# Optimization experiments

Measured on AMD Instinct MI355X. Metric: run time of the kernel, lower is better.

## Reference

```python
import jax, jax.numpy as jnp
import numpy as np

ALPHA = 0.2          # LeakyReLU negative slope
NEG_INF = -9e15      # mask value used by the original module
B, L, D, F_IN, F_OUT = 16, 256, 128, 64, 64


def setup_inputs() -> dict:
    key = jax.random.key(0)
    k1, k2, k3, k4 = jax.random.split(key, 4)
    h = jax.random.normal(k1, (B, L, D, F_IN), dtype=jnp.float32)
    adj = jax.random.randint(k2, (B, L, D, D), 0, 2, dtype=jnp.int32)
    # xavier_uniform(gain=1.414) bounds
    bW = 1.414 * np.sqrt(6.0 / (F_IN + F_OUT))
    W = jax.random.uniform(k3, (F_IN, F_OUT), dtype=jnp.float32, minval=-bW, maxval=bW)
    ba = 1.414 * np.sqrt(6.0 / (2 * F_OUT + 1))
    a = jax.random.uniform(k4, (2 * F_OUT, 1), dtype=jnp.float32, minval=-ba, maxval=ba)
    return {"h": h, "adj": adj, "W": W, "a": a}


def reference(h, adj, W, a):
    # h: [B,L,D,F_in], adj: [B,L,D,D]
    Wh = jnp.einsum('bldf,fo->bldo', h, W)              # [B,L,D,F_out]
    a1 = a[:F_OUT, 0]                                    # dots the "source" node i
    a2 = a[F_OUT:, 0]                                    # dots the "target" node j
    e_i = Wh @ a1                                        # [B,L,D]
    e_j = Wh @ a2                                        # [B,L,D]
    e = e_i[..., :, None] + e_j[..., None, :]            # [B,L,D,D] pairwise scores
    e = jnp.where(e > 0, e, ALPHA * e)                   # LeakyReLU
    att = jnp.where(adj > 0, e, NEG_INF)
    att = jax.nn.softmax(att, axis=-1)                   # dropout=eval mode (no-op)
    h_prime = jnp.einsum('bldk,blko->bldo', att, Wh)     # [B,L,D,F_out]
    return h_prime
```

## Files before the change

### kernel.cpp

```cpp
#include <hip/hip_runtime.h>

constexpr int D_   = 128;
constexpr int FIN  = 64;
constexpr int FOUT = 64;
constexpr float ALPHA = 0.2f;

typedef _Float16 f16x8 __attribute__((ext_vector_type(8)));
typedef float    f32x4 __attribute__((ext_vector_type(4)));

__global__ __launch_bounds__(256, 4) void gat_kernel(
    const float* __restrict__ hg, const int* __restrict__ adjg,
    const float* __restrict__ Wg, const float* __restrict__ ag,
    float* __restrict__ outg)
{
    __shared__ __align__(16) unsigned short sX[128 * 64];
    __shared__ __align__(16) unsigned short sPt[64 * 64];
    __shared__ __align__(16) float sA[2 * FOUT];
    __shared__ float sEi[D_];
    __shared__ __align__(16) float sEj[D_];
    __shared__ float sL[D_];
    __shared__ float sMxW[4];

    const int tid  = threadIdx.x;
    const int lane = tid & 63;
    const int w    = tid >> 6;
    const int g    = lane >> 4;
    const int m16  = lane & 15;

    const long bl = blockIdx.x;
    const float* hp   = hg   + bl * (long)(D_ * FIN);
    const int*   adjp = adjg + bl * (long)(D_ * D_);
    float*       outp = outg + bl * (long)(D_ * FOUT);

    char* xb = (char*)sX;
    char* pb = (char*)sPt;

    {
        const float4* h4 = (const float4*)hp;
        #pragma unroll
        for (int k = 0; k < 8; ++k) {
            int idx = tid + 256 * k;
            float4 v = h4[idx];
            int row = idx >> 4;
            int f   = (idx & 15) << 2;
            union { _Float16 h[4]; uint2 u; } cv;
            cv.h[0] = (_Float16)v.x; cv.h[1] = (_Float16)v.y;
            cv.h[2] = (_Float16)v.z; cv.h[3] = (_Float16)v.w;
            int off = (row * 128 + f * 2) ^ ((row & 7) << 4);
            *(uint2*)(xb + off) = cv.u;
        }
        {
            const int f0 = (tid & 15) * 4;
            const int o0 = (tid >> 4) * 4;
            float4 r0 = *(const float4*)&Wg[(f0 + 0) * 64 + o0];
            float4 r1 = *(const float4*)&Wg[(f0 + 1) * 64 + o0];
            float4 r2 = *(const float4*)&Wg[(f0 + 2) * 64 + o0];
            float4 r3 = *(const float4*)&Wg[(f0 + 3) * 64 + o0];
            float col[4][4] = {{r0.x, r1.x, r2.x, r3.x},
                               {r0.y, r1.y, r2.y, r3.y},
                               {r0.z, r1.z, r2.z, r3.z},
                               {r0.w, r1.w, r2.w, r3.w}};
            #pragma unroll
            for (int c = 0; c < 4; ++c) {
                int o = o0 + c;
                union { _Float16 h[4]; uint2 u; } cv;
                cv.h[0] = (_Float16)col[c][0]; cv.h[1] = (_Float16)col[c][1];
                cv.h[2] = (_Float16)col[c][2]; cv.h[3] = (_Float16)col[c][3];
                int off = (o * 128 + f0 * 2) ^ ((o & 7) << 4);
                *(uint2*)(pb + off) = cv.u;
            }
        }
        if (tid < 2 * FOUT) sA[tid] = ag[tid];
    }

    const int row0 = w * 32 + m16;
    const int* aprow0 = adjp + row0 * D_ + g * 8;
    const int* aprow1 = aprow0 + 16 * D_;
    int4 areg[4];
    areg[0] = *(const int4*)(aprow0);
    areg[1] = *(const int4*)(aprow0 + 4);
    areg[2] = *(const int4*)(aprow1);
    areg[3] = *(const int4*)(aprow1 + 4);
    __syncthreads();

    f32x4 acc[2][4];
    #pragma unroll
    for (int mt = 0; mt < 2; ++mt)
        #pragma unroll
        for (int nt = 0; nt < 4; ++nt) acc[mt][nt] = (f32x4){0.f, 0.f, 0.f, 0.f};

    #pragma unroll
    for (int kt = 0; kt < 2; ++kt) {
        f16x8 af[2], bf[4];
        #pragma unroll
        for (int mt = 0; mt < 2; ++mt) {
            int row = w * 32 + mt * 16 + m16;
            af[mt] = *(const f16x8*)(xb + ((row * 128 + kt * 64 + g * 16) ^ ((row & 7) << 4)));
        }
        #pragma unroll
        for (int nt = 0; nt < 4; ++nt) {
            int o = nt * 16 + m16;
            bf[nt] = *(const f16x8*)(pb + ((o * 128 + kt * 64 + g * 16) ^ ((o & 7) << 4)));
        }
        #pragma unroll
        for (int mt = 0; mt < 2; ++mt)
            #pragma unroll
            for (int nt = 0; nt < 4; ++nt)
                acc[mt][nt] = __builtin_amdgcn_mfma_f32_16x16x32_f16(af[mt], bf[nt], acc[mt][nt], 0, 0, 0);
    }
    __syncthreads();

    {
        float a1v[4], a2v[4];
        #pragma unroll
        for (int nt = 0; nt < 4; ++nt) {
            a1v[nt] = sA[nt * 16 + m16];
            a2v[nt] = sA[FOUT + nt * 16 + m16];
        }
        float wmax = -3.0e38f;
        #pragma unroll
        for (int mt = 0; mt < 2; ++mt) {
            #pragma unroll
            for (int r = 0; r < 4; ++r) {
                float ei = 0.f, ej = 0.f;
                #pragma unroll
                for (int nt = 0; nt < 4; ++nt) {
                    float v = acc[mt][nt][r];
                    ei += v * a1v[nt];
                    ej += v * a2v[nt];
                }
                #pragma unroll
                for (int s = 1; s < 16; s <<= 1) {
                    ei += __shfl_xor(ei, s);
                    ej += __shfl_xor(ej, s);
                }
                int row = w * 32 + mt * 16 + g * 4 + r;
                if (m16 == 0) { sEi[row] = ei; sEj[row] = ej; }
                wmax = fmaxf(wmax, ej);
            }
        }
        wmax = fmaxf(wmax, __shfl_xor(wmax, 16));
        wmax = fmaxf(wmax, __shfl_xor(wmax, 32));
        if (lane == 0) sMxW[w] = wmax;

        #pragma unroll
        for (int mt = 0; mt < 2; ++mt) {
            int j0r = w * 32 + mt * 16 + g * 4;
            #pragma unroll
            for (int nt = 0; nt < 4; ++nt) {
                int o = nt * 16 + m16;
                union { _Float16 h[4]; uint2 u; } cv;
                cv.h[0] = (_Float16)acc[mt][nt][0];
                cv.h[1] = (_Float16)acc[mt][nt][1];
                cv.h[2] = (_Float16)acc[mt][nt][2];
                cv.h[3] = (_Float16)acc[mt][nt][3];
                int off = (o * 256 + j0r * 2) ^ ((o & 7) << 4);
                *(uint2*)(xb + off) = cv.u;
            }
        }
    }
    __syncthreads();

    #pragma unroll
    for (int mt = 0; mt < 2; ++mt)
        #pragma unroll
        for (int nt = 0; nt < 4; ++nt) acc[mt][nt] = (f32x4){0.f, 0.f, 0.f, 0.f};

    const float ei0 = sEi[row0];
    const float ei1 = sEi[row0 + 16];
    const float mxj = fmaxf(fmaxf(sMxW[0], sMxW[1]), fmaxf(sMxW[2], sMxW[3]));
    float t0 = ei0 + mxj, t1 = ei1 + mxj;
    const float mi0 = t0 > 0.f ? t0 : ALPHA * t0;
    const float mi1 = t1 > 0.f ? t1 : ALPHA * t1;
    float lp0 = 0.f, lp1 = 0.f;

    #pragma unroll
    for (int jt = 0; jt < 4; ++jt) {
        const int j0 = jt * 32;
        float4 ejA = *(const float4*)&sEj[j0 + g * 8];
        float4 ejB = *(const float4*)&sEj[j0 + g * 8 + 4];
        float ejv[8] = {ejA.x, ejA.y, ejA.z, ejA.w, ejB.x, ejB.y, ejB.z, ejB.w};
        int aa0[8] = {areg[0].x, areg[0].y, areg[0].z, areg[0].w,
                      areg[1].x, areg[1].y, areg[1].z, areg[1].w};
        int aa1[8] = {areg[2].x, areg[2].y, areg[2].z, areg[2].w,
                      areg[3].x, areg[3].y, areg[3].z, areg[3].w};
        f16x8 pa0, pa1;
        #pragma unroll
        for (int q = 0; q < 8; ++q) {
            float e0 = ei0 + ejv[q];
            e0 = e0 > 0.f ? e0 : ALPHA * e0;
            float p0 = (aa0[q] > 0) ? __expf(e0 - mi0) : 0.f;
            lp0 += p0;
            pa0[q] = (_Float16)p0;
            float e1 = ei1 + ejv[q];
            e1 = e1 > 0.f ? e1 : ALPHA * e1;
            float p1 = (aa1[q] > 0) ? __expf(e1 - mi1) : 0.f;
            lp1 += p1;
            pa1[q] = (_Float16)p1;
        }
        if (jt < 3) {
            const int* n0 = aprow0 + (jt + 1) * 32;
            const int* n1 = aprow1 + (jt + 1) * 32;
            areg[0] = *(const int4*)(n0);
            areg[1] = *(const int4*)(n0 + 4);
            areg[2] = *(const int4*)(n1);
            areg[3] = *(const int4*)(n1 + 4);
        }

        f16x8 wb[4];
        #pragma unroll
        for (int nt = 0; nt < 4; ++nt) {
            int o = nt * 16 + m16;
            wb[nt] = *(const f16x8*)(xb + ((o * 256 + j0 * 2 + g * 16) ^ ((o & 7) << 4)));
        }
        #pragma unroll
        for (int nt = 0; nt < 4; ++nt) {
            acc[0][nt] = __builtin_amdgcn_mfma_f32_16x16x32_f16(pa0, wb[nt], acc[0][nt], 0, 0, 0);
            acc[1][nt] = __builtin_amdgcn_mfma_f32_16x16x32_f16(pa1, wb[nt], acc[1][nt], 0, 0, 0);
        }
    }

    lp0 += __shfl_xor(lp0, 16); lp0 += __shfl_xor(lp0, 32);
    lp1 += __shfl_xor(lp1, 16); lp1 += __shfl_xor(lp1, 32);
    if (g == 0) {
        sL[row0]      = lp0;
        sL[row0 + 16] = lp1;
    }

    #pragma unroll
    for (int mtx = 0; mtx < 2; ++mtx) {
        #pragma unroll
        for (int r = 0; r < 4; ++r) {
            int row = w * 32 + mtx * 16 + g * 4 + r;
            float inv = 1.0f / sL[row];
            #pragma unroll
            for (int nt = 0; nt < 4; ++nt)
                outp[row * 64 + nt * 16 + m16] = acc[mtx][nt][r] * inv;
        }
    }
}

extern "C" void kernel_launch(void* const* d_in, const int* in_sizes, int n_in,
                              void* d_out, int out_size, void* d_ws, size_t ws_size,
                              hipStream_t stream) {
    const float* h   = (const float*)d_in[0];
    const int*   adj = (const int*)d_in[1];
    const float* W   = (const float*)d_in[2];
    const float* a   = (const float*)d_in[3];
    float*       out = (float*)d_out;
    gat_kernel<<<dim3(16 * 256), dim3(256), 0, stream>>>(h, adj, W, a, out);
}
```

Before: 476.0 us.

## Process two (b,l) slices per block with double-buffered h prefetch

Each block now handles two consecutive (b,l) slices, halving the grid. The second slice's h tile is loaded into registers during the first slice's projection, and its adjacency row fragment is prefetched at the end of the first softmax/aggregation phase. W is converted once and shared across both slices. The cost is an extra 16KB of LDS, which may lower occupancy, more register pressure from holding the h prefetch, and fewer blocks to balance across CUs.

```diff
diff --git a/kernel.cpp b/kernel.cpp
--- a/kernel.cpp
+++ b/kernel.cpp
@@ -13,7 +13,8 @@
     const float* __restrict__ Wg, const float* __restrict__ ag,
     float* __restrict__ outg)
 {
-    __shared__ __align__(16) unsigned short sX[128 * 64];
+    __shared__ __align__(16) unsigned short sX0[128 * 64];
+    __shared__ __align__(16) unsigned short sX1[128 * 64];
     __shared__ __align__(16) unsigned short sPt[64 * 64];
     __shared__ __align__(16) float sA[2 * FOUT];
     __shared__ float sEi[D_];
@@ -26,17 +27,26 @@
     const int w    = tid >> 6;
     const int g    = lane >> 4;
     const int m16  = lane & 15;
-
-    const long bl = blockIdx.x;
-    const float* hp   = hg   + bl * (long)(D_ * FIN);
-    const int*   adjp = adjg + bl * (long)(D_ * D_);
-    float*       outp = outg + bl * (long)(D_ * FOUT);
-
-    char* xb = (char*)sX;
-    char* pb = (char*)sPt;
+    const int row0 = w * 32 + m16;
+
+    const long bl0 = 2 * (long)blockIdx.x;
+    const long bl1 = bl0 + 1;
+    const float* hp0   = hg   + bl0 * (long)(D_ * FIN);
+    const float* hp1   = hg   + bl1 * (long)(D_ * FIN);
+    const int*   adjp0 = adjg + bl0 * (long)(D_ * D_);
+    const int*   adjp1 = adjg + bl1 * (long)(D_ * D_);
+    float*       outp0 = outg + bl0 * (long)(D_ * FOUT);
+    float*       outp1 = outg + bl1 * (long)(D_ * FOUT);
+
+    char* xb0 = (char*)sX0;
+    char* xb1 = (char*)sX1;
+    char* pb  = (char*)sPt;
+
+    f32x4 acc[2][4];
+    int4  areg[4];
 
     {
-        const float4* h4 = (const float4*)hp;
+        const float4* h4 = (const float4*)hp0;
         #pragma unroll
         for (int k = 0; k < 8; ++k) {
             int idx = tid + 256 * k;
@@ -47,70 +57,63 @@
             cv.h[0] = (_Float16)v.x; cv.h[1] = (_Float16)v.y;
             cv.h[2] = (_Float16)v.z; cv.h[3] = (_Float16)v.w;
             int off = (row * 128 + f * 2) ^ ((row & 7) << 4);
-            *(uint2*)(xb + off) = cv.u;
-        }
-        {
-            const int f0 = (tid & 15) * 4;
-            const int o0 = (tid >> 4) * 4;
-            float4 r0 = *(const float4*)&Wg[(f0 + 0) * 64 + o0];
-            float4 r1 = *(const float4*)&Wg[(f0 + 1) * 64 + o0];
-            float4 r2 = *(const float4*)&Wg[(f0 + 2) * 64 + o0];
-            float4 r3 = *(const float4*)&Wg[(f0 + 3) * 64 + o0];
-            float col[4][4] = {{r0.x, r1.x, r2.x, r3.x},
-                               {r0.y, r1.y, r2.y, r3.y},
-                               {r0.z, r1.z, r2.z, r3.z},
-                               {r0.w, r1.w, r2.w, r3.w}};
-            #pragma unroll
-            for (int c = 0; c < 4; ++c) {
-                int o = o0 + c;
-                union { _Float16 h[4]; uint2 u; } cv;
-                cv.h[0] = (_Float16)col[c][0]; cv.h[1] = (_Float16)col[c][1];
-                cv.h[2] = (_Float16)col[c][2]; cv.h[3] = (_Float16)col[c][3];
-                int off = (o * 128 + f0 * 2) ^ ((o & 7) << 4);
-                *(uint2*)(pb + off) = cv.u;
-            }
+            *(uint2*)(xb0 + off) = cv.u;
+        }
+        const int f0 = (tid & 15) * 4;
+        const int o0 = (tid >> 4) * 4;
+        float4 r0 = *(const float4*)&Wg[(f0 + 0) * 64 + o0];
+        float4 r1 = *(const float4*)&Wg[(f0 + 1) * 64 + o0];
+        float4 r2 = *(const float4*)&Wg[(f0 + 2) * 64 + o0];
+        float4 r3 = *(const float4*)&Wg[(f0 + 3) * 64 + o0];
+        float col[4][4] = {{r0.x, r1.x, r2.x, r3.x},
+                           {r0.y, r1.y, r2.y, r3.y},
+                           {r0.z, r1.z, r2.z, r3.z},
+                           {r0.w, r1.w, r2.w, r3.w}};
+        #pragma unroll
+        for (int c = 0; c < 4; ++c) {
+            int o = o0 + c;
+            union { _Float16 h[4]; uint2 u; } cv;
+            cv.h[0] = (_Float16)col[c][0]; cv.h[1] = (_Float16)col[c][1];
+            cv.h[2] = (_Float16)col[c][2]; cv.h[3] = (_Float16)col[c][3];
+            int off = (o * 128 + f0 * 2) ^ ((o & 7) << 4);
+            *(uint2*)(pb + off) = cv.u;
         }
         if (tid < 2 * FOUT) sA[tid] = ag[tid];
+        const int* a0 = adjp0 + row0 * D_ + g * 8;
+        areg[0] = *(const int4*)(a0);
+        areg[1] = *(const int4*)(a0 + 4);
+        areg[2] = *(const int4*)(a0 + 16 * D_);
+        areg[3] = *(const int4*)(a0 + 16 * D_ + 4);
     }
-
-    const int row0 = w * 32 + m16;
-    const int* aprow0 = adjp + row0 * D_ + g * 8;
-    const int* aprow1 = aprow0 + 16 * D_;
-    int4 areg[4];
-    areg[0] = *(const int4*)(aprow0);
-    areg[1] = *(const int4*)(aprow0 + 4);
-    areg[2] = *(const int4*)(aprow1);
-    areg[3] = *(const int4*)(aprow1 + 4);
-    __syncthreads();
-
-    f32x4 acc[2][4];
-    #pragma unroll
-    for (int mt = 0; mt < 2; ++mt)
-        #pragma unroll
-        for (int nt = 0; nt < 4; ++nt) acc[mt][nt] = (f32x4){0.f, 0.f, 0.f, 0.f};
-
-    #pragma unroll
-    for (int kt = 0; kt < 2; ++kt) {
-        f16x8 af[2], bf[4];
-        #pragma unroll
-        for (int mt = 0; mt < 2; ++mt) {
-            int row = w * 32 + mt * 16 + m16;
-            af[mt] = *(const f16x8*)(xb + ((row * 128 + kt * 64 + g * 16) ^ ((row & 7) << 4)));
-        }
-        #pragma unroll
-        for (int nt = 0; nt < 4; ++nt) {
-            int o = nt * 16 + m16;
-            bf[nt] = *(const f16x8*)(pb + ((o * 128 + kt * 64 + g * 16) ^ ((o & 7) << 4)));
-        }
+    __syncthreads();
+
+    auto phaseA = [&](char* xb) {
         #pragma unroll
         for (int mt = 0; mt < 2; ++mt)
             #pragma unroll
-            for (int nt = 0; nt < 4; ++nt)
-                acc[mt][nt] = __builtin_amdgcn_mfma_f32_16x16x32_f16(af[mt], bf[nt], acc[mt][nt], 0, 0, 0);
-    }
-    __syncthreads();
-
-    {
+            for (int nt = 0; nt < 4; ++nt) acc[mt][nt] = (f32x4){0.f, 0.f, 0.f, 0.f};
+        #pragma unroll
+        for (int kt = 0; kt < 2; ++kt) {
+            f16x8 af[2], bf[4];
+            #pragma unroll
+            for (int mt = 0; mt < 2; ++mt) {
+                int row = w * 32 + mt * 16 + m16;
+                af[mt] = *(const f16x8*)(xb + ((row * 128 + kt * 64 + g * 16) ^ ((row & 7) << 4)));
+            }
+            #pragma unroll
+            for (int nt = 0; nt < 4; ++nt) {
+                int o = nt * 16 + m16;
+                bf[nt] = *(const f16x8*)(pb + ((o * 128 + kt * 64 + g * 16) ^ ((o & 7) << 4)));
+            }
+            #pragma unroll
+            for (int mt = 0; mt < 2; ++mt)
+                #pragma unroll
+                for (int nt = 0; nt < 4; ++nt)
+                    acc[mt][nt] = __builtin_amdgcn_mfma_f32_16x16x32_f16(af[mt], bf[nt], acc[mt][nt], 0, 0, 0);
+        }
+    };
+
+    auto phaseB = [&](char* xb) {
         float a1v[4], a2v[4];
         #pragma unroll
         for (int nt = 0; nt < 4; ++nt) {
@@ -142,7 +145,6 @@
         wmax = fmaxf(wmax, __shfl_xor(wmax, 16));
         wmax = fmaxf(wmax, __shfl_xor(wmax, 32));
         if (lane == 0) sMxW[w] = wmax;
-
         #pragma unroll
         for (int mt = 0; mt < 2; ++mt) {
             int j0r = w * 32 + mt * 16 + g * 4;
@@ -158,86 +160,121 @@
                 *(uint2*)(xb + off) = cv.u;
             }
         }
+    };
+
+    auto phaseC = [&](char* xb, const int* adjp, float* outp, const int* adjp_next) {
+        #pragma unroll
+        for (int mt = 0; mt < 2; ++mt)
+            #pragma unroll
+            for (int nt = 0; nt < 4; ++nt) acc[mt][nt] = (f32x4){0.f, 0.f, 0.f, 0.f};
+        const float ei0 = sEi[row0];
+        const float ei1 = sEi[row0 + 16];
+        const float mxj = fmaxf(fmaxf(sMxW[0], sMxW[1]), fmaxf(sMxW[2], sMxW[3]));
+        float t0 = ei0 + mxj, t1 = ei1 + mxj;
+        const float mi0 = t0 > 0.f ? t0 : ALPHA * t0;
+        const float mi1 = t1 > 0.f ? t1 : ALPHA * t1;
+        float lp0 = 0.f, lp1 = 0.f;
+        const int* aprow0 = adjp + row0 * D_ + g * 8;
+        const int* aprow1 = aprow0 + 16 * D_;
+        #pragma unroll
+        for (int jt = 0; jt < 4; ++jt) {
+            const int j0 = jt * 32;
+            float4 ejA = *(const float4*)&sEj[j0 + g * 8];
+            float4 ejB = *(const float4*)&sEj[j0 + g * 8 + 4];
+            float ejv[8] = {ejA.x, ejA.y, ejA.z, ejA.w, ejB.x, ejB.y, ejB.z, ejB.w};
+            int aa0[8] = {areg[0].x, areg[0].y, areg[0].z, areg[0].w,
+                          areg[1].x, areg[1].y, areg[1].z, areg[1].w};
+            int aa1[8] = {areg[2].x, areg[2].y, areg[2].z, areg[2].w,
+                          areg[3].x, areg[3].y, areg[3].z, areg[3].w};
+            f16x8 pa0, pa1;
+            #pragma unroll
+            for (int q = 0; q < 8; ++q) {
+                float e0 = ei0 + ejv[q];
+                e0 = e0 > 0.f ? e0 : ALPHA * e0;
+                float p0 = (aa0[q] > 0) ? __expf(e0 - mi0) : 0.f;
+                lp0 += p0;
+                pa0[q] = (_Float16)p0;
+                float e1 = ei1 + ejv[q];
+                e1 = e1 > 0.f ? e1 : ALPHA * e1;
+                float p1 = (aa1[q] > 0) ? __expf(e1 - mi1) : 0.f;
+                lp1 += p1;
+                pa1[q] = (_Float16)p1;
+            }
+            if (jt < 3) {
+                const int* n0 = aprow0 + (jt + 1) * 32;
+                const int* n1 = aprow1 + (jt + 1) * 32;
+                areg[0] = *(const int4*)(n0);
+                areg[1] = *(const int4*)(n0 + 4);
+                areg[2] = *(const int4*)(n1);
+                areg[3] = *(const int4*)(n1 + 4);
+            } else if (adjp_next) {
+                const int* n0 = adjp_next + row0 * D_ + g * 8;
+                areg[0] = *(const int4*)(n0);
+                areg[1] = *(const int4*)(n0 + 4);
+                areg[2] = *(const int4*)(n0 + 16 * D_);
+                areg[3] = *(const int4*)(n0 + 16 * D_ + 4);
+            }
+            f16x8 wb[4];
+            #pragma unroll
+            for (int nt = 0; nt < 4; ++nt) {
+                int o = nt * 16 + m16;
+                wb[nt] = *(const f16x8*)(xb + ((o * 256 + j0 * 2 + g * 16) ^ ((o & 7) << 4)));
+            }
+            #pragma unroll
+            for (int nt = 0; nt < 4; ++nt) {
+                acc[0][nt] = __builtin_amdgcn_mfma_f32_16x16x32_f16(pa0, wb[nt], acc[0][nt], 0, 0, 0);
+                acc[1][nt] = __builtin_amdgcn_mfma_f32_16x16x32_f16(pa1, wb[nt], acc[1][nt], 0, 0, 0);
+            }
+        }
+        lp0 += __shfl_xor(lp0, 16); lp0 += __shfl_xor(lp0, 32);
+        lp1 += __shfl_xor(lp1, 16); lp1 += __shfl_xor(lp1, 32);
+        if (g == 0) {
+            sL[row0]      = lp0;
+            sL[row0 + 16] = lp1;
+        }
+        #pragma unroll
+        for (int mtx = 0; mtx < 2; ++mtx) {
+            #pragma unroll
+            for (int r = 0; r < 4; ++r) {
+                int row = w * 32 + mtx * 16 + g * 4 + r;
+                float inv = 1.0f / sL[row];
+                #pragma unroll
+                for (int nt = 0; nt < 4; ++nt)
+                    outp[row * 64 + nt * 16 + m16] = acc[mtx][nt][r] * inv;
+            }
+        }
+    };
+
+    phaseA(xb0);
+    float4 hreg[8];
+    {
+        const float4* h4 = (const float4*)hp1;
+        #pragma unroll
+        for (int k = 0; k < 8; ++k) hreg[k] = h4[tid + 256 * k];
     }
     __syncthreads();
-
+    phaseB(xb0);
     #pragma unroll
-    for (int mt = 0; mt < 2; ++mt)
-        #pragma unroll
-        for (int nt = 0; nt < 4; ++nt) acc[mt][nt] = (f32x4){0.f, 0.f, 0.f, 0.f};
-
-    const float ei0 = sEi[row0];
-    const float ei1 = sEi[row0 + 16];
-    const float mxj = fmaxf(fmaxf(sMxW[0], sMxW[1]), fmaxf(sMxW[2], sMxW[3]));
-    float t0 = ei0 + mxj, t1 = ei1 + mxj;
-    const float mi0 = t0 > 0.f ? t0 : ALPHA * t0;
-    const float mi1 = t1 > 0.f ? t1 : ALPHA * t1;
-    float lp0 = 0.f, lp1 = 0.f;
-
-    #pragma unroll
-    for (int jt = 0; jt < 4; ++jt) {
-        const int j0 = jt * 32;
-        float4 ejA = *(const float4*)&sEj[j0 + g * 8];
-        float4 ejB = *(const float4*)&sEj[j0 + g * 8 + 4];
-        float ejv[8] = {ejA.x, ejA.y, ejA.z, ejA.w, ejB.x, ejB.y, ejB.z, ejB.w};
-        int aa0[8] = {areg[0].x, areg[0].y, areg[0].z, areg[0].w,
-                      areg[1].x, areg[1].y, areg[1].z, areg[1].w};
-        int aa1[8] = {areg[2].x, areg[2].y, areg[2].z, areg[2].w,
-                      areg[3].x, areg[3].y, areg[3].z, areg[3].w};
-        f16x8 pa0, pa1;
-        #pragma unroll
-        for (int q = 0; q < 8; ++q) {
-            float e0 = ei0 + ejv[q];
-            e0 = e0 > 0.f ? e0 : ALPHA * e0;
-            float p0 = (aa0[q] > 0) ? __expf(e0 - mi0) : 0.f;
-            lp0 += p0;
-            pa0[q] = (_Float16)p0;
-            float e1 = ei1 + ejv[q];
-            e1 = e1 > 0.f ? e1 : ALPHA * e1;
-            float p1 = (aa1[q] > 0) ? __expf(e1 - mi1) : 0.f;
-            lp1 += p1;
-            pa1[q] = (_Float16)p1;
-        }
-        if (jt < 3) {
-            const int* n0 = aprow0 + (jt + 1) * 32;
-            const int* n1 = aprow1 + (jt + 1) * 32;
-            areg[0] = *(const int4*)(n0);
-            areg[1] = *(const int4*)(n0 + 4);
-            areg[2] = *(const int4*)(n1);
-            areg[3] = *(const int4*)(n1 + 4);
-        }
-
-        f16x8 wb[4];
-        #pragma unroll
-        for (int nt = 0; nt < 4; ++nt) {
-            int o = nt * 16 + m16;
-            wb[nt] = *(const f16x8*)(xb + ((o * 256 + j0 * 2 + g * 16) ^ ((o & 7) << 4)));
-        }
-        #pragma unroll
-        for (int nt = 0; nt < 4; ++nt) {
-            acc[0][nt] = __builtin_amdgcn_mfma_f32_16x16x32_f16(pa0, wb[nt], acc[0][nt], 0, 0, 0);
-            acc[1][nt] = __builtin_amdgcn_mfma_f32_16x16x32_f16(pa1, wb[nt], acc[1][nt], 0, 0, 0);
-        }
+    for (int k = 0; k < 8; ++k) {
+        int idx = tid + 256 * k;
+        float4 v = hreg[k];
+        int row = idx >> 4;
+        int f   = (idx & 15) << 2;
+        union { _Float16 h[4]; uint2 u; } cv;
+        cv.h[0] = (_Float16)v.x; cv.h[1] = (_Float16)v.y;
+        cv.h[2] = (_Float16)v.z; cv.h[3] = (_Float16)v.w;
+        int off = (row * 128 + f * 2) ^ ((row & 7) << 4);
+        *(uint2*)(xb1 + off) = cv.u;
     }
-
-    lp0 += __shfl_xor(lp0, 16); lp0 += __shfl_xor(lp0, 32);
-    lp1 += __shfl_xor(lp1, 16); lp1 += __shfl_xor(lp1, 32);
-    if (g == 0) {
-        sL[row0]      = lp0;
-        sL[row0 + 16] = lp1;
-    }
-
-    #pragma unroll
-    for (int mtx = 0; mtx < 2; ++mtx) {
-        #pragma unroll
-        for (int r = 0; r < 4; ++r) {
-            int row = w * 32 + mtx * 16 + g * 4 + r;
-            float inv = 1.0f / sL[row];
-            #pragma unroll
-            for (int nt = 0; nt < 4; ++nt)
-                outp[row * 64 + nt * 16 + m16] = acc[mtx][nt][r] * inv;
-        }
-    }
+    __syncthreads();
+    phaseC(xb0, adjp0, outp0, adjp1);
+
+    __syncthreads();
+    phaseA(xb1);
+    __syncthreads();
+    phaseB(xb1);
+    __syncthreads();
+    phaseC(xb1, adjp1, outp1, nullptr);
 }
 
 extern "C" void kernel_launch(void* const* d_in, const int* in_sizes, int n_in,
@@ -248,5 +285,5 @@
     const float* W   = (const float*)d_in[2];
     const float* a   = (const float*)d_in[3];
     float*       out = (float*)d_out;
-    gat_kernel<<<dim3(16 * 256), dim3(256), 0, stream>>>(h, adj, W, a, out);
+    gat_kernel<<<dim3(16 * 256 / 2), dim3(256), 0, stream>>>(h, adj, W, a, out);
 }
```

Result: no change. 473.3 us (-0.6%).

## Load h directly into MFMA A-fragments, drop sPt and sA shared buffers

Applied to the files above, without the earlier changes.

Each wave now loads its h rows straight from global memory into registers as f16 MFMA A-operands, so h is no longer staged through shared memory. The transposed W is written into the sX buffer that h used to occupy, and the attention vector a is read directly from global memory, which removes the sPt and sA shared arrays. The aim is to cut LDS footprint (for better occupancy) and LDS traffic in the first GEMM. In exchange, global loads of h are less coalesced (32 B per lane, strided by row), and sX is reused for Wh later, so correctness depends on the existing barrier placement.

```diff
diff --git a/kernel.cpp b/kernel.cpp
--- a/kernel.cpp
+++ b/kernel.cpp
@@ -14,8 +14,6 @@
     float* __restrict__ outg)
 {
     __shared__ __align__(16) unsigned short sX[128 * 64];
-    __shared__ __align__(16) unsigned short sPt[64 * 64];
-    __shared__ __align__(16) float sA[2 * FOUT];
     __shared__ float sEi[D_];
     __shared__ __align__(16) float sEj[D_];
     __shared__ float sL[D_];
@@ -26,6 +24,7 @@
     const int w    = tid >> 6;
     const int g    = lane >> 4;
     const int m16  = lane & 15;
+    const int row0 = w * 32 + m16;
 
     const long bl = blockIdx.x;
     const float* hp   = hg   + bl * (long)(D_ * FIN);
@@ -33,56 +32,58 @@
     float*       outp = outg + bl * (long)(D_ * FOUT);
 
     char* xb = (char*)sX;
-    char* pb = (char*)sPt;
-
+
+    f16x8 ha[2][2];
+    #pragma unroll
+    for (int mt = 0; mt < 2; ++mt)
+        #pragma unroll
+        for (int kt = 0; kt < 2; ++kt) {
+            const float* hb = hp + (w * 32 + mt * 16 + m16) * 64 + kt * 32 + g * 8;
+            float4 v0 = *(const float4*)hb;
+            float4 v1 = *(const float4*)(hb + 4);
+            ha[mt][kt][0] = (_Float16)v0.x; ha[mt][kt][1] = (_Float16)v0.y;
+            ha[mt][kt][2] = (_Float16)v0.z; ha[mt][kt][3] = (_Float16)v0.w;
+            ha[mt][kt][4] = (_Float16)v1.x; ha[mt][kt][5] = (_Float16)v1.y;
+            ha[mt][kt][6] = (_Float16)v1.z; ha[mt][kt][7] = (_Float16)v1.w;
+        }
+    int4 areg[4];
     {
-        const float4* h4 = (const float4*)hp;
-        #pragma unroll
-        for (int k = 0; k < 8; ++k) {
-            int idx = tid + 256 * k;
-            float4 v = h4[idx];
-            int row = idx >> 4;
-            int f   = (idx & 15) << 2;
+        const int* a0 = adjp + row0 * D_ + g * 8;
+        areg[0] = *(const int4*)(a0);
+        areg[1] = *(const int4*)(a0 + 4);
+        areg[2] = *(const int4*)(a0 + 16 * D_);
+        areg[3] = *(const int4*)(a0 + 16 * D_ + 4);
+    }
+    {
+        const int f0 = (tid & 15) * 4;
+        const int o0 = (tid >> 4) * 4;
+        float4 r0 = *(const float4*)&Wg[(f0 + 0) * 64 + o0];
+        float4 r1 = *(const float4*)&Wg[(f0 + 1) * 64 + o0];
+        float4 r2 = *(const float4*)&Wg[(f0 + 2) * 64 + o0];
+        float4 r3 = *(const float4*)&Wg[(f0 + 3) * 64 + o0];
+        float col[4][4] = {{r0.x, r1.x, r2.x, r3.x}, {r0.y, r1.y, r2.y, r3.y},
+                           {r0.z, r1.z, r2.z, r3.z}, {r0.w, r1.w, r2.w, r3.w}};
+        #pragma unroll
+        for (int c = 0; c < 4; ++c) {
+            int o = o0 + c;
             union { _Float16 h[4]; uint2 u; } cv;
-            cv.h[0] = (_Float16)v.x; cv.h[1] = (_Float16)v.y;
-            cv.h[2] = (_Float16)v.z; cv.h[3] = (_Float16)v.w;
-            int off = (row * 128 + f * 2) ^ ((row & 7) << 4);
+            cv.h[0] = (_Float16)col[c][0]; cv.h[1] = (_Float16)col[c][1];
+            cv.h[2] = (_Float16)col[c][2]; cv.h[3] = (_Float16)col[c][3];
+            int off = (o * 128 + f0 * 2) ^ ((o & 7) << 4);
             *(uint2*)(xb + off) = cv.u;
         }
-        {
-            const int f0 = (tid & 15) * 4;
-            const int o0 = (tid >> 4) * 4;
-            float4 r0 = *(const float4*)&Wg[(f0 + 0) * 64 + o0];
-            float4 r1 = *(const float4*)&Wg[(f0 + 1) * 64 + o0];
-            float4 r2 = *(const float4*)&Wg[(f0 + 2) * 64 + o0];
-            float4 r3 = *(const float4*)&Wg[(f0 + 3) * 64 + o0];
-            float col[4][4] = {{r0.x, r1.x, r2.x, r3.x},
-                               {r0.y, r1.y, r2.y, r3.y},
-                               {r0.z, r1.z, r2.z, r3.z},
-                               {r0.w, r1.w, r2.w, r3.w}};
-            #pragma unroll
-            for (int c = 0; c < 4; ++c) {
-                int o = o0 + c;
-                union { _Float16 h[4]; uint2 u; } cv;
-                cv.h[0] = (_Float16)col[c][0]; cv.h[1] = (_Float16)col[c][1];
-                cv.h[2] = (_Float16)col[c][2]; cv.h[3] = (_Float16)col[c][3];
-                int off = (o * 128 + f0 * 2) ^ ((o & 7) << 4);
-                *(uint2*)(pb + off) = cv.u;
-            }
-        }
-        if (tid < 2 * FOUT) sA[tid] = ag[tid];
-    }
-
-    const int row0 = w * 32 + m16;
-    const int* aprow0 = adjp + row0 * D_ + g * 8;
-    const int* aprow1 = aprow0 + 16 * D_;
-    int4 areg[4];
-    areg[0] = *(const int4*)(aprow0);
-    areg[1] = *(const int4*)(aprow0 + 4);
-    areg[2] = *(const int4*)(aprow1);
-    areg[3] = *(const int4*)(aprow1 + 4);
+    }
     __syncthreads();
 
+    f16x8 wf[2][4];
+    #pragma unroll
+    for (int kt = 0; kt < 2; ++kt)
+        #pragma unroll
+        for (int nt = 0; nt < 4; ++nt) {
+            int o = nt * 16 + m16;
+            wf[kt][nt] = *(const f16x8*)(xb + ((o * 128 + kt * 64 + g * 16) ^ ((o & 7) << 4)));
+        }
+
     f32x4 acc[2][4];
     #pragma unroll
     for (int mt = 0; mt < 2; ++mt)
@@ -90,32 +91,20 @@
         for (int nt = 0; nt < 4; ++nt) acc[mt][nt] = (f32x4){0.f, 0.f, 0.f, 0.f};
 
     #pragma unroll
-    for (int kt = 0; kt < 2; ++kt) {
-        f16x8 af[2], bf[4];
-        #pragma unroll
-        for (int mt = 0; mt < 2; ++mt) {
-            int row = w * 32 + mt * 16 + m16;
-            af[mt] = *(const f16x8*)(xb + ((row * 128 + kt * 64 + g * 16) ^ ((row & 7) << 4)));
-        }
-        #pragma unroll
-        for (int nt = 0; nt < 4; ++nt) {
-            int o = nt * 16 + m16;
-            bf[nt] = *(const f16x8*)(pb + ((o * 128 + kt * 64 + g * 16) ^ ((o & 7) << 4)));
-        }
+    for (int kt = 0; kt < 2; ++kt)
         #pragma unroll
         for (int mt = 0; mt < 2; ++mt)
             #pragma unroll
             for (int nt = 0; nt < 4; ++nt)
-                acc[mt][nt] = __builtin_amdgcn_mfma_f32_16x16x32_f16(af[mt], bf[nt], acc[mt][nt], 0, 0, 0);
-    }
+                acc[mt][nt] = __builtin_amdgcn_mfma_f32_16x16x32_f16(ha[mt][kt], wf[kt][nt], acc[mt][nt], 0, 0, 0);
     __syncthreads();
 
     {
         float a1v[4], a2v[4];
         #pragma unroll
         for (int nt = 0; nt < 4; ++nt) {
-            a1v[nt] = sA[nt * 16 + m16];
-            a2v[nt] = sA[FOUT + nt * 16 + m16];
+            a1v[nt] = ag[nt * 16 + m16];
+            a2v[nt] = ag[FOUT + nt * 16 + m16];
         }
         float wmax = -3.0e38f;
         #pragma unroll
@@ -174,6 +163,9 @@
     const float mi1 = t1 > 0.f ? t1 : ALPHA * t1;
     float lp0 = 0.f, lp1 = 0.f;
 
+    const int* aprow0 = adjp + row0 * D_ + g * 8;
+    const int* aprow1 = aprow0 + 16 * D_;
+
     #pragma unroll
     for (int jt = 0; jt < 4; ++jt) {
         const int j0 = jt * 32;
@@ -206,7 +198,6 @@
             areg[2] = *(const int4*)(n1);
             areg[3] = *(const int4*)(n1 + 4);
         }
-
         f16x8 wb[4];
         #pragma unroll
         for (int nt = 0; nt < 4; ++nt) {
```

Result: no change. 473.9 us (-0.5%).
